# Performance work log

Hardware: AMD Instinct MI355X
Metric: run time of the kernel (lower is better)

The kernel has to match this reference:

```python
import jax, jax.numpy as jnp
import numpy as np

D = 512
H = 8
DH = D // H
SPK = 4
HG = 128  # max(16, D//4)
EPS = 1e-5


def _layernorm(x, gamma, beta):
    mu = jnp.mean(x, axis=-1, keepdims=True)
    var = jnp.var(x, axis=-1, keepdims=True)
    return (x - mu) * jax.lax.rsqrt(var + EPS) * gamma + beta


def setup_inputs() -> dict:
    key = jax.random.key(0)
    ks = jax.random.split(key, 16)
    B, T = 8, 4096
    s = 0.02
    return {
        'token_emb': jax.random.normal(ks[0], (B, T, D), jnp.float32),
        'speaker_emb': jax.random.normal(ks[1], (B, D), jnp.float32),
        'We': jax.random.normal(ks[2], (D * SPK, D), jnp.float32) * s,
        'be': jnp.zeros((D * SPK,), jnp.float32),
        'spk_pos': jax.random.normal(ks[3], (1, SPK, D), jnp.float32) * s,
        'Wq': jax.random.normal(ks[4], (D, D), jnp.float32) * s,
        'bq': jnp.zeros((D,), jnp.float32),
        'Wk': jax.random.normal(ks[5], (D, D), jnp.float32) * s,
        'bk': jnp.zeros((D,), jnp.float32),
        'Wv': jax.random.normal(ks[6], (D, D), jnp.float32) * s,
        'bv': jnp.zeros((D,), jnp.float32),
        'Wo': jax.random.normal(ks[7], (D, D), jnp.float32) * s,
        'bo': jnp.zeros((D,), jnp.float32),
        'gln_gamma': jnp.ones((D,), jnp.float32),
        'gln_beta': jnp.zeros((D,), jnp.float32),
        'Wg1': jax.random.normal(ks[8], (HG, D), jnp.float32) * s,
        'bg1': jnp.zeros((HG,), jnp.float32),
        'Wg2': jax.random.normal(ks[9], (1, HG), jnp.float32) * s,
        'bg2': jnp.zeros((1,), jnp.float32),
        'ln_gamma': jnp.ones((D,), jnp.float32),
        'ln_beta': jnp.zeros((D,), jnp.float32),
    }


def reference(token_emb, speaker_emb, We, be, spk_pos, Wq, bq, Wk, bk, Wv, bv,
              Wo, bo, gln_gamma, gln_beta, Wg1, bg1, Wg2, bg2, ln_gamma, ln_beta):
    B, T, _ = token_emb.shape
    # speaker expansion: (B,D) -> (B, SPK*D) -> (B,SPK,D), plus learned pos
    spk_tokens = jax.nn.relu(speaker_emb @ We.T + be).reshape(B, SPK, D) + spk_pos
    # multi-head cross-attention (batch_first, eval-mode dropout = identity)
    q = (token_emb @ Wq.T + bq).reshape(B, T, H, DH)
    k = (spk_tokens @ Wk.T + bk).reshape(B, SPK, H, DH)
    v = (spk_tokens @ Wv.T + bv).reshape(B, SPK, H, DH)
    scores = jnp.einsum('bthd,bshd->bhts', q, k) / jnp.sqrt(jnp.float32(DH))
    w = jax.nn.softmax(scores, axis=-1)  # (B,H,T,SPK)
    ctx = jnp.einsum('bhts,bshd->bthd', w, v).reshape(B, T, D)
    attn_output = ctx @ Wo.T + bo
    attn_weights = jnp.mean(w, axis=1)  # torch MHA averages heads -> (B,T,SPK)
    # gate: LN -> Linear -> ReLU -> Linear -> Sigmoid
    g = _layernorm(token_emb, gln_gamma, gln_beta)
    g = jax.nn.relu(g @ Wg1.T + bg1)
    g_used = jax.nn.sigmoid(g @ Wg2.T + bg2)  # (B,T,1)
    # residual + final LayerNorm (dropout identity in eval)
    fused = _layernorm(token_emb + g_used * attn_output, ln_gamma, ln_beta)
    return (fused, attn_weights, g_used)
```

## Files before the change

kernel.cpp:

```cpp
#include <hip/hip_runtime.h>
#include <hip/hip_bf16.h>
#include <stdint.h>

typedef __attribute__((ext_vector_type(8))) short short8;
typedef __attribute__((ext_vector_type(4))) short short4v;
typedef __attribute__((ext_vector_type(4))) float f32x4;
typedef __attribute__((ext_vector_type(2))) unsigned int uint2v;

#define DD 512
#define TT 16
#define TN 4096
#define NB 8

__device__ __forceinline__ unsigned short f2bf(float f){
  uint32_t u = __float_as_uint(f);
  u += 0x7FFFu + ((u >> 16) & 1u);
  return (unsigned short)(u >> 16);
}
__device__ __forceinline__ float bf2f(unsigned short h){
  return __uint_as_float(((uint32_t)h) << 16);
}


__global__ void prep_spk(const float* __restrict__ se, const float* __restrict__ We,
                         const float* __restrict__ be, const float* __restrict__ spos,
                         float* __restrict__ spk){
  int idx = blockIdx.x * 256 + threadIdx.x;
  int sub = idx & 15; int out = idx >> 4;
  int b = out & 7, od = out >> 3;
  const float* wr = We + (size_t)od * DD + sub * 4;
  const float* sb = se + b * DD + sub * 4;
  float acc = 0.f;
#pragma unroll
  for (int i = 0; i < 8; i++){
    float4 w = *(const float4*)(wr + i * 64);
    float4 x = *(const float4*)(sb + i * 64);
    acc += w.x * x.x + w.y * x.y + w.z * x.z + w.w * x.w;
  }
  acc += __shfl_xor(acc, 1); acc += __shfl_xor(acc, 2);
  acc += __shfl_xor(acc, 4); acc += __shfl_xor(acc, 8);
  if (sub == 0) spk[b * 2048 + od] = fmaxf(acc + be[od], 0.f) + spos[od];
}

__global__ void prep_kv(const float* __restrict__ spk, const float* __restrict__ Wk,
                        const float* __restrict__ bk, const float* __restrict__ Wv,
                        const float* __restrict__ bv, float* __restrict__ kb,
                        float* __restrict__ vb){
  int idx = blockIdx.x * 256 + threadIdx.x;
  int sub = idx & 15; int out = idx >> 4;
  int hd = out >> 5; int r = out & 31; int b = r >> 2, s = r & 3;
  const float* sp  = spk + (b * 4 + s) * DD + sub * 4;
  const float* wkr = Wk + (size_t)hd * DD + sub * 4;
  const float* wvr = Wv + (size_t)hd * DD + sub * 4;
  float ak = 0.f, av = 0.f;
#pragma unroll
  for (int i = 0; i < 8; i++){
    float4 x  = *(const float4*)(sp + i * 64);
    float4 wk = *(const float4*)(wkr + i * 64);
    float4 wv = *(const float4*)(wvr + i * 64);
    ak += x.x * wk.x + x.y * wk.y + x.z * wk.z + x.w * wk.w;
    av += x.x * wv.x + x.y * wv.y + x.z * wv.z + x.w * wv.w;
  }
  ak += __shfl_xor(ak, 1); ak += __shfl_xor(ak, 2);
  ak += __shfl_xor(ak, 4); ak += __shfl_xor(ak, 8);
  av += __shfl_xor(av, 1); av += __shfl_xor(av, 2);
  av += __shfl_xor(av, 4); av += __shfl_xor(av, 8);
  if (sub == 0){
    kb[(b * 4 + s) * DD + hd] = ak + bk[hd];
    vb[(b * 4 + s) * DD + hd] = av + bv[hd];
  }
}

__global__ void prep_mu(const float* __restrict__ kb, const float* __restrict__ vb,
                        const float* __restrict__ Wq, const float* __restrict__ bq,
                        const float* __restrict__ Wo, const float* __restrict__ bo,
                        const float* __restrict__ Wg1,
                        const float* __restrict__ glng, const float* __restrict__ glnb,
                        const float* __restrict__ bg1,
                        unsigned short* __restrict__ mS, unsigned short* __restrict__ uS,
                        float* __restrict__ cArr, unsigned short* __restrict__ wg1S,
                        float* __restrict__ e1, float* __restrict__ e2){
  int idx = blockIdx.x * 256 + threadIdx.x;
  if (idx < 131072){
    int d = idx & 511; int j = (idx >> 9) & 31; int b = idx >> 14;
    int h = j >> 2, s = j & 3;
    const float* kr = kb + (b * 4 + s) * DD + h * 64;
    const float* wq = Wq + (size_t)(h * 64) * DD + d;
    float acc = 0.f;
#pragma unroll 16
    for (int dh = 0; dh < 64; dh++) acc += wq[(size_t)dh * DD] * kr[dh];
    int kt = d >> 5, kgp = (d >> 3) & 3, e = d & 7;
    int half = j >> 4;
    mS[(size_t)(b * 16 + kt) * 1024 + half * 512 + (kgp * 16 + (j & 15)) * 8 + e] = f2bf(acc);
  } else if (idx < 262144){
    int t = idx - 131072;
    int j = t & 31; int d = (t >> 5) & 511; int b = t >> 14;
    int h = j >> 2, s = j & 3;
    const float* vr = vb + (b * 4 + s) * DD + h * 64;
    const float* wo = Wo + (size_t)d * DD + h * 64;
    float acc = 0.f;
#pragma unroll 8
    for (int dh = 0; dh < 64; dh += 4){
      float4 v4 = *(const float4*)(vr + dh);
      float4 w4 = *(const float4*)(wo + dh);
      acc += v4.x * w4.x + v4.y * w4.y + v4.z * w4.z + v4.w * w4.w;
    }
    int nc = d >> 7, nt = (d >> 4) & 7, r16p = d & 15;
    int kgp = j >> 3, e = j & 7;
    uS[(size_t)(b * 32 + nc * 8 + nt) * 512 + (kgp * 16 + r16p) * 8 + e] =
        f2bf(acc + bo[d] * 0.125f);
  } else if (idx < 327680){
    int t = idx - 262144;
    int col = t >> 9, d = t & 511;
    int nt = col >> 4, c16 = col & 15;
    int kt = d >> 5, kgp = (d >> 3) & 3, e = d & 7;
    wg1S[(size_t)(nt * 16 + kt) * 512 + (kgp * 16 + c16) * 8 + e] = f2bf(Wg1[t] * glng[d]);
  } else if (idx < 327936){
    int t = idx - 327680; int j = t & 31, b = t >> 5;
    int h = j >> 2, s = j & 3;
    const float* kr = kb + (b * 4 + s) * DD + h * 64;
    const float* bqp = bq + h * 64;
    float acc = 0.f;
    for (int dh = 0; dh < 64; dh++) acc += bqp[dh] * kr[dh];
    cArr[b * 32 + j] = acc;
  } else if (idx < 328064){
    int col = idx - 327936;
    const float* wr = Wg1 + (size_t)col * DD;
    float a1 = 0.f, a2 = 0.f;
    for (int d = 0; d < DD; d += 4){
      float4 w  = *(const float4*)(wr + d);
      float4 gm = *(const float4*)(glng + d);
      float4 bt = *(const float4*)(glnb + d);
      a1 += w.x * gm.x + w.y * gm.y + w.z * gm.z + w.w * gm.w;
      a2 += w.x * bt.x + w.y * bt.y + w.z * bt.z + w.w * bt.w;
    }
    e1[col] = a1; e2[col] = a2 + bg1[col];
  }
}


__global__ __launch_bounds__(64) void fused_main(
    const float* __restrict__ xin,
    const float* __restrict__ e1v, const float* __restrict__ e2v,
    const float* __restrict__ wg2v, const float* __restrict__ bg2v,
    const float* __restrict__ lng, const float* __restrict__ lnb,
    const unsigned short* __restrict__ mS,
    const unsigned short* __restrict__ uS,
    const float* __restrict__ cArr,
    const unsigned short* __restrict__ wg1S,
    float* __restrict__ outF, float* __restrict__ outAW, float* __restrict__ outG)
{
  __shared__ __align__(16) unsigned short Yb[TT * DD];
  __shared__ __align__(16) unsigned short Wl[TT * 32];

  const int lane = threadIdx.x;
  const int r16 = lane & 15;
  const int kg  = lane >> 4;
  const int bb  = blockIdx.x >> 8;
  const int t0  = (blockIdx.x & 255) << 4;
  const size_t rowbase = (size_t)bb * TN + t0;
  const int swzS = (r16 & 7) << 3;

  const float* xbase = xin + rowbase * DD;
  float4 xl[32];
#pragma unroll
  for (int i = 0; i < 32; i++){
    const int r = i >> 1;
    xl[i] = *(const float4*)(xbase + r * DD + (i & 1) * 256 + lane * 4);
  }
#pragma unroll
  for (int i = 0; i < 32; i++){
    const int r = i >> 1;
    const int col = (i & 1) * 256 + lane * 4;
    short4v pk;
    pk[0] = (short)f2bf(xl[i].x); pk[1] = (short)f2bf(xl[i].y);
    pk[2] = (short)f2bf(xl[i].z); pk[3] = (short)f2bf(xl[i].w);
    *(short4v*)&Yb[r * DD + (col ^ ((r & 7) << 3))] = pk;
  }
  __syncthreads();

  short8 af[16];
  float s = 0.f, q = 0.f;
#pragma unroll
  for (int kt = 0; kt < 16; kt++){
    af[kt] = *(const short8*)&Yb[r16 * DD + ((kt * 32 + kg * 8) ^ swzS)];
#pragma unroll
    for (int j = 0; j < 8; j++){
      float v = bf2f((unsigned short)af[kt][j]);
      s += v; q += v * v;
    }
  }
  s += __shfl_xor(s, 16); s += __shfl_xor(s, 32);
  q += __shfl_xor(q, 16); q += __shfl_xor(q, 32);
  const float mu = s * (1.f / DD);
  const float rs = rsqrtf(q * (1.f / DD) - mu * mu + 1e-5f);

  const unsigned short* mSp = mS + (size_t)bb * 16384;
  f32x4 sa0 = {0.f,0.f,0.f,0.f}, sa1 = {0.f,0.f,0.f,0.f};
  f32x4 gacc[8];
#pragma unroll
  for (int nt = 0; nt < 8; nt++){ f32x4 z = {0.f,0.f,0.f,0.f}; gacc[nt] = z; }
#pragma unroll
  for (int kt = 0; kt < 16; kt++){
    short8 b0 = *(const short8*)(mSp + (size_t)kt * 1024 + lane * 8);
    short8 b1 = *(const short8*)(mSp + (size_t)kt * 1024 + 512 + lane * 8);
    sa0 = __builtin_amdgcn_mfma_f32_16x16x32_bf16(af[kt], b0, sa0, 0, 0, 0);
    sa1 = __builtin_amdgcn_mfma_f32_16x16x32_bf16(af[kt], b1, sa1, 0, 0, 0);
#pragma unroll
    for (int nt = 0; nt < 8; nt++){
      short8 wf = *(const short8*)(wg1S + (size_t)(nt * 16 + kt) * 512 + lane * 8);
      gacc[nt] = __builtin_amdgcn_mfma_f32_16x16x32_bf16(wf, af[kt], gacc[nt], 0, 0, 0);
    }
  }

  float4 e1c[8], e2c[8], w2c[8];
#pragma unroll
  for (int nt = 0; nt < 8; nt++){
    const int c4 = nt * 16 + kg * 4;
    e1c[nt] = *(const float4*)(e1v + c4);
    e2c[nt] = *(const float4*)(e2v + c4);
    w2c[nt] = *(const float4*)(wg2v + c4);
  }
  const float c0v  = cArr[bb * 32 + r16];
  const float c1v  = cArr[bb * 32 + r16 + 16];
  const float bg2s = bg2v[0];

#pragma unroll
  for (int r = 0; r < 4; r++){
    float s0 = (sa0[r] + c0v) * 0.125f;
    float s1 = (sa1[r] + c1v) * 0.125f;
    float mx0 = fmaxf(s0, __shfl_xor(s0, 1)); mx0 = fmaxf(mx0, __shfl_xor(mx0, 2));
    float mx1 = fmaxf(s1, __shfl_xor(s1, 1)); mx1 = fmaxf(mx1, __shfl_xor(mx1, 2));
    float e0 = __expf(s0 - mx0), e1x = __expf(s1 - mx1);
    float d0 = e0;  d0 += __shfl_xor(d0, 1); d0 += __shfl_xor(d0, 2);
    float d1 = e1x; d1 += __shfl_xor(d1, 1); d1 += __shfl_xor(d1, 2);
    float w0 = e0 / d0, w1 = e1x / d1;
    float t = w0 + w1; t += __shfl_xor(t, 4); t += __shfl_xor(t, 8); t *= 0.125f;
    const int rw = kg * 4 + r;
    if ((lane & 12) == 0) outAW[(rowbase + rw) * 4 + (lane & 3)] = t;
    Wl[rw * 32 + r16]      = f2bf(w0);
    Wl[rw * 32 + r16 + 16] = f2bf(w1);
  }

  short8 aw = *(const short8*)&Wl[r16 * 32 + kg * 8];
  const unsigned short* uSp = uS + (size_t)bb * 16384;
  const int c0 = lane << 3;
  float4 lgA0 = *(const float4*)(lng + c0);
  float4 lgA1 = *(const float4*)(lng + c0 + 4);
  float4 lbA0 = *(const float4*)(lnb + c0);
  float4 lbA1 = *(const float4*)(lnb + c0 + 4);

  float g_reg;
  {
    float part = 0.f;
#pragma unroll
    for (int nt = 0; nt < 8; nt++){
      float e1a[4] = {e1c[nt].x, e1c[nt].y, e1c[nt].z, e1c[nt].w};
      float e2a[4] = {e2c[nt].x, e2c[nt].y, e2c[nt].z, e2c[nt].w};
      float w2a[4] = {w2c[nt].x, w2c[nt].y, w2c[nt].z, w2c[nt].w};
#pragma unroll
      for (int r = 0; r < 4; r++){
        float gv = rs * (gacc[nt][r] - mu * e1a[r]) + e2a[r];
        gv = fmaxf(gv, 0.f);
        part += gv * w2a[r];
      }
    }
    part += __shfl_xor(part, 16); part += __shfl_xor(part, 32);
    g_reg = 1.f / (1.f + __expf(-(part + bg2s)));
    if (kg == 0) outG[rowbase + r16] = g_reg;
  }

  float psum = 0.f, psq = 0.f;
#pragma unroll
  for (int nc = 0; nc < 4; nc++){
    f32x4 acc[8];
#pragma unroll
    for (int nt = 0; nt < 8; nt++){
      short8 uf = *(const short8*)(uSp + (size_t)(nc * 8 + nt) * 512 + lane * 8);
      f32x4 z = {0.f,0.f,0.f,0.f};
      acc[nt] = __builtin_amdgcn_mfma_f32_16x16x32_bf16(uf, aw, z, 0, 0, 0);
    }
#pragma unroll
    for (int nt = 0; nt < 8; nt++){
      const int idx = r16 * DD + ((nc * 128 + nt * 16 + kg * 4) ^ swzS);
      uint2v xch = *(const uint2v*)&Yb[idx];
      unsigned int lo = xch[0], hi = xch[1];
      float y0 = bf2f((unsigned short)(lo & 0xffffu)) + g_reg * acc[nt][0];
      float y1 = bf2f((unsigned short)(lo >> 16))     + g_reg * acc[nt][1];
      float y2 = bf2f((unsigned short)(hi & 0xffffu)) + g_reg * acc[nt][2];
      float y3 = bf2f((unsigned short)(hi >> 16))     + g_reg * acc[nt][3];
      psum += (y0 + y1) + (y2 + y3);
      psq  += (y0 * y0 + y1 * y1) + (y2 * y2 + y3 * y3);
      uint2v yp;
      yp[0] = (unsigned)f2bf(y0) | ((unsigned)f2bf(y1) << 16);
      yp[1] = (unsigned)f2bf(y2) | ((unsigned)f2bf(y3) << 16);
      *(uint2v*)&Yb[idx] = yp;
    }
  }

  psum += __shfl_xor(psum, 16); psum += __shfl_xor(psum, 32);
  psq  += __shfl_xor(psq, 16);  psq  += __shfl_xor(psq, 32);
  const float mu2 = psum * (1.f / DD);
  const float rs2 = rsqrtf(psq * (1.f / DD) - mu2 * mu2 + 1e-5f);

  float lg[8]  = {lgA0.x, lgA0.y, lgA0.z, lgA0.w, lgA1.x, lgA1.y, lgA1.z, lgA1.w};
  float lb8[8] = {lbA0.x, lbA0.y, lbA0.z, lbA0.w, lbA1.x, lbA1.y, lbA1.z, lbA1.w};
#pragma unroll
  for (int r = 0; r < TT; r++){
    const float m2  = __shfl(mu2, r);
    const float r2v = __shfl(rs2, r);
    short8 yv = *(const short8*)&Yb[r * DD + (c0 ^ ((r & 7) << 3))];
    float o[8];
#pragma unroll
    for (int j = 0; j < 8; j++)
      o[j] = (bf2f((unsigned short)yv[j]) - m2) * r2v * lg[j] + lb8[j];
    float* op = outF + (rowbase + r) * DD + c0;
    float4 o0; o0.x = o[0]; o0.y = o[1]; o0.z = o[2]; o0.w = o[3];
    float4 o1; o1.x = o[4]; o1.y = o[5]; o1.z = o[6]; o1.w = o[7];
    *(float4*)op = o0;
    *(float4*)(op + 4) = o1;
  }
}


extern "C" void kernel_launch(void* const* d_in, const int* in_sizes, int n_in,
                              void* d_out, int out_size, void* d_ws, size_t ws_size,
                              hipStream_t stream)
{
  const float* token = (const float*)d_in[0];
  const float* semb  = (const float*)d_in[1];
  const float* We    = (const float*)d_in[2];
  const float* be    = (const float*)d_in[3];
  const float* spos  = (const float*)d_in[4];
  const float* Wq    = (const float*)d_in[5];
  const float* bq    = (const float*)d_in[6];
  const float* Wk    = (const float*)d_in[7];
  const float* bk    = (const float*)d_in[8];
  const float* Wv    = (const float*)d_in[9];
  const float* bv    = (const float*)d_in[10];
  const float* Wo    = (const float*)d_in[11];
  const float* bo    = (const float*)d_in[12];
  const float* glng  = (const float*)d_in[13];
  const float* glnb  = (const float*)d_in[14];
  const float* Wg1   = (const float*)d_in[15];
  const float* bg1   = (const float*)d_in[16];
  const float* Wg2   = (const float*)d_in[17];
  const float* bg2   = (const float*)d_in[18];
  const float* lng   = (const float*)d_in[19];
  const float* lnb   = (const float*)d_in[20];

  char* ws = (char*)d_ws;
  float* e1             = (float*)(ws + 0);
  float* e2             = (float*)(ws + 512);
  float* spk            = (float*)(ws + 0);
  float* kb             = (float*)(ws + 65536);
  float* vb             = (float*)(ws + 131072);
  unsigned short* mS    = (unsigned short*)(ws + 196608);
  unsigned short* uS    = (unsigned short*)(ws + 458752);
  float* cArr           = (float*)(ws + 720896);
  unsigned short* wg1S  = (unsigned short*)(ws + 721920);

  float* outF  = (float*)d_out;
  float* outAW = outF + (size_t)NB * TN * DD;
  float* outG  = outAW + (size_t)NB * TN * 4;

  prep_spk<<<dim3(1024), dim3(256), 0, stream>>>(semb, We, be, spos, spk);
  prep_kv<<<dim3(1024), dim3(256), 0, stream>>>(spk, Wk, bk, Wv, bv, kb, vb);
  prep_mu<<<dim3(1282), dim3(256), 0, stream>>>(kb, vb, Wq, bq, Wo, bo, Wg1, glng, glnb, bg1,
                                                mS, uS, cArr, wg1S, e1, e2);
  fused_main<<<dim3(NB * TN / TT), dim3(64), 0, stream>>>(
      token, e1, e2, Wg2, bg2, lng, lnb,
      mS, uS, cArr, wg1S, outF, outAW, outG);
}
```

Before: 71.58 us.

## Split fused main kernel across four waves and merge prep kernels

The main kernel moves from one 64-thread wave per 16-token tile to four waves. The waves share the score, gate and Wo-projection MFMAs, and LayerNorm statistics are combined through shared memory with extra barriers. The three prep kernels become two: speaker expansion, K/V projection and the bias dot run in 32 blocks using shared memory, and the Wg1 packing is done per wave. The goal is less serial work and fewer registers per wave (the old xl[32] and af[16] arrays are gone) so occupancy rises, at the cost of more syncs and shared-memory traffic per block.

```diff
diff --git a/kernel.cpp b/kernel.cpp
--- a/kernel.cpp
+++ b/kernel.cpp
@@ -22,64 +22,101 @@
 }
 
 
-__global__ void prep_spk(const float* __restrict__ se, const float* __restrict__ We,
-                         const float* __restrict__ be, const float* __restrict__ spos,
-                         float* __restrict__ spk){
-  int idx = blockIdx.x * 256 + threadIdx.x;
-  int sub = idx & 15; int out = idx >> 4;
-  int b = out & 7, od = out >> 3;
-  const float* wr = We + (size_t)od * DD + sub * 4;
-  const float* sb = se + b * DD + sub * 4;
-  float acc = 0.f;
-#pragma unroll
-  for (int i = 0; i < 8; i++){
-    float4 w = *(const float4*)(wr + i * 64);
-    float4 x = *(const float4*)(sb + i * 64);
-    acc += w.x * x.x + w.y * x.y + w.z * x.z + w.w * x.w;
-  }
-  acc += __shfl_xor(acc, 1); acc += __shfl_xor(acc, 2);
-  acc += __shfl_xor(acc, 4); acc += __shfl_xor(acc, 8);
-  if (sub == 0) spk[b * 2048 + od] = fmaxf(acc + be[od], 0.f) + spos[od];
-}
-
-__global__ void prep_kv(const float* __restrict__ spk, const float* __restrict__ Wk,
-                        const float* __restrict__ bk, const float* __restrict__ Wv,
-                        const float* __restrict__ bv, float* __restrict__ kb,
-                        float* __restrict__ vb){
-  int idx = blockIdx.x * 256 + threadIdx.x;
-  int sub = idx & 15; int out = idx >> 4;
-  int hd = out >> 5; int r = out & 31; int b = r >> 2, s = r & 3;
-  const float* sp  = spk + (b * 4 + s) * DD + sub * 4;
-  const float* wkr = Wk + (size_t)hd * DD + sub * 4;
-  const float* wvr = Wv + (size_t)hd * DD + sub * 4;
-  float ak = 0.f, av = 0.f;
-#pragma unroll
-  for (int i = 0; i < 8; i++){
-    float4 x  = *(const float4*)(sp + i * 64);
-    float4 wk = *(const float4*)(wkr + i * 64);
-    float4 wv = *(const float4*)(wvr + i * 64);
-    ak += x.x * wk.x + x.y * wk.y + x.z * wk.z + x.w * wk.w;
-    av += x.x * wv.x + x.y * wv.y + x.z * wv.z + x.w * wv.w;
-  }
-  ak += __shfl_xor(ak, 1); ak += __shfl_xor(ak, 2);
-  ak += __shfl_xor(ak, 4); ak += __shfl_xor(ak, 8);
-  av += __shfl_xor(av, 1); av += __shfl_xor(av, 2);
-  av += __shfl_xor(av, 4); av += __shfl_xor(av, 8);
-  if (sub == 0){
-    kb[(b * 4 + s) * DD + hd] = ak + bk[hd];
-    vb[(b * 4 + s) * DD + hd] = av + bv[hd];
-  }
-}
-
-__global__ void prep_mu(const float* __restrict__ kb, const float* __restrict__ vb,
-                        const float* __restrict__ Wq, const float* __restrict__ bq,
-                        const float* __restrict__ Wo, const float* __restrict__ bo,
-                        const float* __restrict__ Wg1,
-                        const float* __restrict__ glng, const float* __restrict__ glnb,
-                        const float* __restrict__ bg1,
-                        unsigned short* __restrict__ mS, unsigned short* __restrict__ uS,
-                        float* __restrict__ cArr, unsigned short* __restrict__ wg1S,
-                        float* __restrict__ e1, float* __restrict__ e2){
+__global__ __launch_bounds__(256) void prep_a(
+    const float* __restrict__ se, const float* __restrict__ We,
+    const float* __restrict__ be, const float* __restrict__ spos,
+    const float* __restrict__ Wk, const float* __restrict__ bk,
+    const float* __restrict__ Wv, const float* __restrict__ bv,
+    const float* __restrict__ bq, const float* __restrict__ Wg1,
+    const float* __restrict__ glng, const float* __restrict__ glnb,
+    const float* __restrict__ bg1,
+    float* __restrict__ kb, float* __restrict__ vb,
+    float* __restrict__ cArr, unsigned short* __restrict__ wg1S,
+    float* __restrict__ e1, float* __restrict__ e2)
+{
+  const int blk = blockIdx.x, tid = threadIdx.x;
+  if (blk < 32){
+    __shared__ float spk_loc[512];
+    __shared__ float k_loc[512], v_loc[512];
+    const int b = blk >> 2, s = blk & 3;
+    const int sub = tid & 3, o0 = tid >> 2;
+    const float* sb = se + b * DD + sub * 4;
+#pragma unroll
+    for (int pass = 0; pass < 8; ++pass){
+      const int o = pass * 64 + o0;
+      const float* wr = We + (size_t)(s * DD + o) * DD + sub * 4;
+      float acc = 0.f;
+#pragma unroll
+      for (int i = 0; i < 32; ++i){
+        float4 w4 = *(const float4*)(wr + i * 16);
+        float4 x4 = *(const float4*)(sb + i * 16);
+        acc += w4.x*x4.x + w4.y*x4.y + w4.z*x4.z + w4.w*x4.w;
+      }
+      acc += __shfl_xor(acc, 1); acc += __shfl_xor(acc, 2);
+      if (sub == 0) spk_loc[o] = fmaxf(acc + be[s*DD+o], 0.f) + spos[s*DD+o];
+    }
+    __syncthreads();
+#pragma unroll
+    for (int pass = 0; pass < 8; ++pass){
+      const int hd = pass * 64 + o0;
+      const float* wkr = Wk + (size_t)hd * DD + sub * 4;
+      const float* wvr = Wv + (size_t)hd * DD + sub * 4;
+      float ak = 0.f, av = 0.f;
+#pragma unroll
+      for (int i = 0; i < 32; ++i){
+        float4 x4  = *(const float4*)(&spk_loc[sub*4 + i*16]);
+        float4 wk4 = *(const float4*)(wkr + i * 16);
+        float4 wv4 = *(const float4*)(wvr + i * 16);
+        ak += x4.x*wk4.x + x4.y*wk4.y + x4.z*wk4.z + x4.w*wk4.w;
+        av += x4.x*wv4.x + x4.y*wv4.y + x4.z*wv4.z + x4.w*wv4.w;
+      }
+      ak += __shfl_xor(ak, 1); ak += __shfl_xor(ak, 2);
+      av += __shfl_xor(av, 1); av += __shfl_xor(av, 2);
+      if (sub == 0){
+        const float kk = ak + bk[hd], vv = av + bv[hd];
+        k_loc[hd] = kk; v_loc[hd] = vv;
+        kb[(b*4+s)*DD + hd] = kk; vb[(b*4+s)*DD + hd] = vv;
+      }
+    }
+    __syncthreads();
+    if (tid < 8){
+      float acc = 0.f;
+      for (int dh = 0; dh < 64; ++dh) acc += bq[tid*64+dh] * k_loc[tid*64+dh];
+      cArr[b*32 + tid*4 + s] = acc;
+    }
+  } else {
+    const int wv = tid >> 6, lane = tid & 63;
+    const int col = (blk - 32) * 4 + wv;
+    const float* wr = Wg1 + (size_t)col * DD + lane * 8;
+    float4 w0 = *(const float4*)wr, w1 = *(const float4*)(wr + 4);
+    float4 g0 = *(const float4*)(glng + lane*8), g1 = *(const float4*)(glng + lane*8 + 4);
+    float4 b0 = *(const float4*)(glnb + lane*8), b1 = *(const float4*)(glnb + lane*8 + 4);
+    float wa[8] = {w0.x,w0.y,w0.z,w0.w,w1.x,w1.y,w1.z,w1.w};
+    float ga[8] = {g0.x,g0.y,g0.z,g0.w,g1.x,g1.y,g1.z,g1.w};
+    float ba[8] = {b0.x,b0.y,b0.z,b0.w,b1.x,b1.y,b1.z,b1.w};
+    float p1 = 0.f, p2 = 0.f;
+    short8 st;
+#pragma unroll
+    for (int j = 0; j < 8; ++j){
+      p1 += wa[j]*ga[j]; p2 += wa[j]*ba[j];
+      st[j] = (short)f2bf(wa[j]*ga[j]);
+    }
+    *(short8*)&wg1S[((size_t)((col>>4)*16 + (lane>>2)))*512 + ((lane&3)*16 + (col&15))*8] = st;
+#pragma unroll
+    for (int off = 1; off < 64; off <<= 1){
+      p1 += __shfl_xor(p1, off); p2 += __shfl_xor(p2, off);
+    }
+    if (lane == 0){ e1[col] = p1; e2[col] = p2 + bg1[col]; }
+  }
+}
+
+
+__global__ __launch_bounds__(256) void prep_b(
+    const float* __restrict__ kb, const float* __restrict__ vb,
+    const float* __restrict__ Wq, const float* __restrict__ Wo,
+    const float* __restrict__ bo,
+    unsigned short* __restrict__ mS, unsigned short* __restrict__ uS)
+{
   int idx = blockIdx.x * 256 + threadIdx.x;
   if (idx < 131072){
     int d = idx & 511; int j = (idx >> 9) & 31; int b = idx >> 14;
@@ -92,7 +129,7 @@
     int kt = d >> 5, kgp = (d >> 3) & 3, e = d & 7;
     int half = j >> 4;
     mS[(size_t)(b * 16 + kt) * 1024 + half * 512 + (kgp * 16 + (j & 15)) * 8 + e] = f2bf(acc);
-  } else if (idx < 262144){
+  } else {
     int t = idx - 131072;
     int j = t & 31; int d = (t >> 5) & 511; int b = t >> 14;
     int h = j >> 2, s = j & 3;
@@ -109,37 +146,11 @@
     int kgp = j >> 3, e = j & 7;
     uS[(size_t)(b * 32 + nc * 8 + nt) * 512 + (kgp * 16 + r16p) * 8 + e] =
         f2bf(acc + bo[d] * 0.125f);
-  } else if (idx < 327680){
-    int t = idx - 262144;
-    int col = t >> 9, d = t & 511;
-    int nt = col >> 4, c16 = col & 15;
-    int kt = d >> 5, kgp = (d >> 3) & 3, e = d & 7;
-    wg1S[(size_t)(nt * 16 + kt) * 512 + (kgp * 16 + c16) * 8 + e] = f2bf(Wg1[t] * glng[d]);
-  } else if (idx < 327936){
-    int t = idx - 327680; int j = t & 31, b = t >> 5;
-    int h = j >> 2, s = j & 3;
-    const float* kr = kb + (b * 4 + s) * DD + h * 64;
-    const float* bqp = bq + h * 64;
-    float acc = 0.f;
-    for (int dh = 0; dh < 64; dh++) acc += bqp[dh] * kr[dh];
-    cArr[b * 32 + j] = acc;
-  } else if (idx < 328064){
-    int col = idx - 327936;
-    const float* wr = Wg1 + (size_t)col * DD;
-    float a1 = 0.f, a2 = 0.f;
-    for (int d = 0; d < DD; d += 4){
-      float4 w  = *(const float4*)(wr + d);
-      float4 gm = *(const float4*)(glng + d);
-      float4 bt = *(const float4*)(glnb + d);
-      a1 += w.x * gm.x + w.y * gm.y + w.z * gm.z + w.w * gm.w;
-      a2 += w.x * bt.x + w.y * bt.y + w.z * bt.z + w.w * bt.w;
-    }
-    e1[col] = a1; e2[col] = a2 + bg1[col];
-  }
-}
-
-
-__global__ __launch_bounds__(64) void fused_main(
+  }
+}
+
+
+__global__ __launch_bounds__(256, 4) void fused_main(
     const float* __restrict__ xin,
     const float* __restrict__ e1v, const float* __restrict__ e2v,
     const float* __restrict__ wg2v, const float* __restrict__ bg2v,
@@ -152,173 +163,192 @@
 {
   __shared__ __align__(16) unsigned short Yb[TT * DD];
   __shared__ __align__(16) unsigned short Wl[TT * 32];
-
-  const int lane = threadIdx.x;
-  const int r16 = lane & 15;
-  const int kg  = lane >> 4;
-  const int bb  = blockIdx.x >> 8;
-  const int t0  = (blockIdx.x & 255) << 4;
+  __shared__ float smu[TT], srs[TT];
+  __shared__ float aws[2][64];
+  __shared__ float gp[4][TT];
+  __shared__ float pp[4][TT], qq[4][TT];
+
+  const int tid  = threadIdx.x;
+  const int w    = tid >> 6;
+  const int lane = tid & 63;
+  const int r16  = lane & 15;
+  const int kg   = lane >> 4;
+  const int bb   = blockIdx.x >> 8;
+  const int t0   = (blockIdx.x & 255) << 4;
   const size_t rowbase = (size_t)bb * TN + t0;
   const int swzS = (r16 & 7) << 3;
 
   const float* xbase = xin + rowbase * DD;
-  float4 xl[32];
-#pragma unroll
-  for (int i = 0; i < 32; i++){
-    const int r = i >> 1;
-    xl[i] = *(const float4*)(xbase + r * DD + (i & 1) * 256 + lane * 4);
-  }
-#pragma unroll
-  for (int i = 0; i < 32; i++){
-    const int r = i >> 1;
-    const int col = (i & 1) * 256 + lane * 4;
-    short4v pk;
-    pk[0] = (short)f2bf(xl[i].x); pk[1] = (short)f2bf(xl[i].y);
-    pk[2] = (short)f2bf(xl[i].z); pk[3] = (short)f2bf(xl[i].w);
-    *(short4v*)&Yb[r * DD + (col ^ ((r & 7) << 3))] = pk;
+#pragma unroll
+  for (int i = 0; i < 4; ++i){
+    const int rr = w * 4 + i;
+    const int swz = (rr & 7) << 3;
+    float s = 0.f, q = 0.f;
+#pragma unroll
+    for (int h2 = 0; h2 < 2; ++h2){
+      const int col = h2 * 256 + lane * 4;
+      float4 v4 = *(const float4*)(xbase + rr * DD + col);
+      float xv[4] = {v4.x, v4.y, v4.z, v4.w};
+      short4v pk;
+#pragma unroll
+      for (int j = 0; j < 4; ++j){ s += xv[j]; q += xv[j]*xv[j]; pk[j] = (short)f2bf(xv[j]); }
+      *(short4v*)&Yb[rr * DD + (col ^ swz)] = pk;
+    }
+#pragma unroll
+    for (int off = 1; off < 64; off <<= 1){ s += __shfl_xor(s, off); q += __shfl_xor(q, off); }
+    if (lane == 0){
+      const float mu = s * (1.f/DD);
+      smu[rr] = mu;
+      srs[rr] = rsqrtf(q * (1.f/DD) - mu*mu + 1e-5f);
+    }
   }
   __syncthreads();
 
-  short8 af[16];
-  float s = 0.f, q = 0.f;
-#pragma unroll
-  for (int kt = 0; kt < 16; kt++){
-    af[kt] = *(const short8*)&Yb[r16 * DD + ((kt * 32 + kg * 8) ^ swzS)];
-#pragma unroll
-    for (int j = 0; j < 8; j++){
-      float v = bf2f((unsigned short)af[kt][j]);
-      s += v; q += v * v;
-    }
-  }
-  s += __shfl_xor(s, 16); s += __shfl_xor(s, 32);
-  q += __shfl_xor(q, 16); q += __shfl_xor(q, 32);
-  const float mu = s * (1.f / DD);
-  const float rs = rsqrtf(q * (1.f / DD) - mu * mu + 1e-5f);
-
-  const unsigned short* mSp = mS + (size_t)bb * 16384;
-  f32x4 sa0 = {0.f,0.f,0.f,0.f}, sa1 = {0.f,0.f,0.f,0.f};
-  f32x4 gacc[8];
-#pragma unroll
-  for (int nt = 0; nt < 8; nt++){ f32x4 z = {0.f,0.f,0.f,0.f}; gacc[nt] = z; }
-#pragma unroll
-  for (int kt = 0; kt < 16; kt++){
-    short8 b0 = *(const short8*)(mSp + (size_t)kt * 1024 + lane * 8);
-    short8 b1 = *(const short8*)(mSp + (size_t)kt * 1024 + 512 + lane * 8);
-    sa0 = __builtin_amdgcn_mfma_f32_16x16x32_bf16(af[kt], b0, sa0, 0, 0, 0);
-    sa1 = __builtin_amdgcn_mfma_f32_16x16x32_bf16(af[kt], b1, sa1, 0, 0, 0);
-#pragma unroll
-    for (int nt = 0; nt < 8; nt++){
-      short8 wf = *(const short8*)(wg1S + (size_t)(nt * 16 + kt) * 512 + lane * 8);
-      gacc[nt] = __builtin_amdgcn_mfma_f32_16x16x32_bf16(wf, af[kt], gacc[nt], 0, 0, 0);
-    }
-  }
-
-  float4 e1c[8], e2c[8], w2c[8];
-#pragma unroll
-  for (int nt = 0; nt < 8; nt++){
-    const int c4 = nt * 16 + kg * 4;
-    e1c[nt] = *(const float4*)(e1v + c4);
-    e2c[nt] = *(const float4*)(e2v + c4);
-    w2c[nt] = *(const float4*)(wg2v + c4);
-  }
-  const float c0v  = cArr[bb * 32 + r16];
-  const float c1v  = cArr[bb * 32 + r16 + 16];
+  const int half = w & 1;
+  const int nt0 = w * 2;
+  const unsigned short* mSp  = mS + (size_t)bb * 16384 + half * 512 + lane * 8;
+  const unsigned short* wgp0 = wg1S + (size_t)(nt0 * 16) * 512 + lane * 8;
+  const unsigned short* wgp1 = wgp0 + (size_t)16 * 512;
+  f32x4 sa = {0.f,0.f,0.f,0.f}, ga0 = {0.f,0.f,0.f,0.f}, ga1 = {0.f,0.f,0.f,0.f};
+  if (w < 2){
+#pragma unroll
+    for (int kt = 0; kt < 16; ++kt){
+      short8 af = *(const short8*)&Yb[r16 * DD + ((kt*32 + kg*8) ^ swzS)];
+      short8 b0 = *(const short8*)(mSp + (size_t)kt * 1024);
+      sa  = __builtin_amdgcn_mfma_f32_16x16x32_bf16(af, b0, sa, 0, 0, 0);
+      short8 wf0 = *(const short8*)(wgp0 + (size_t)kt * 512);
+      ga0 = __builtin_amdgcn_mfma_f32_16x16x32_bf16(wf0, af, ga0, 0, 0, 0);
+      short8 wf1 = *(const short8*)(wgp1 + (size_t)kt * 512);
+      ga1 = __builtin_amdgcn_mfma_f32_16x16x32_bf16(wf1, af, ga1, 0, 0, 0);
+    }
+  } else {
+#pragma unroll
+    for (int kt = 0; kt < 16; ++kt){
+      short8 af = *(const short8*)&Yb[r16 * DD + ((kt*32 + kg*8) ^ swzS)];
+      short8 wf0 = *(const short8*)(wgp0 + (size_t)kt * 512);
+      ga0 = __builtin_amdgcn_mfma_f32_16x16x32_bf16(wf0, af, ga0, 0, 0, 0);
+      short8 wf1 = *(const short8*)(wgp1 + (size_t)kt * 512);
+      ga1 = __builtin_amdgcn_mfma_f32_16x16x32_bf16(wf1, af, ga1, 0, 0, 0);
+    }
+  }
+
+  float4 e1c[2], e2c[2], w2c[2];
+#pragma unroll
+  for (int t = 0; t < 2; ++t){
+    const int c4 = (nt0 + t) * 16 + kg * 4;
+    e1c[t] = *(const float4*)(e1v + c4);
+    e2c[t] = *(const float4*)(e2v + c4);
+    w2c[t] = *(const float4*)(wg2v + c4);
+  }
+  float4 lgh[2], lbh[2];
+#pragma unroll
+  for (int h2 = 0; h2 < 2; ++h2){
+    lgh[h2] = *(const float4*)(lng + h2*256 + lane*4);
+    lbh[h2] = *(const float4*)(lnb + h2*256 + lane*4);
+  }
   const float bg2s = bg2v[0];
 
-#pragma unroll
-  for (int r = 0; r < 4; r++){
-    float s0 = (sa0[r] + c0v) * 0.125f;
-    float s1 = (sa1[r] + c1v) * 0.125f;
-    float mx0 = fmaxf(s0, __shfl_xor(s0, 1)); mx0 = fmaxf(mx0, __shfl_xor(mx0, 2));
-    float mx1 = fmaxf(s1, __shfl_xor(s1, 1)); mx1 = fmaxf(mx1, __shfl_xor(mx1, 2));
-    float e0 = __expf(s0 - mx0), e1x = __expf(s1 - mx1);
-    float d0 = e0;  d0 += __shfl_xor(d0, 1); d0 += __shfl_xor(d0, 2);
-    float d1 = e1x; d1 += __shfl_xor(d1, 1); d1 += __shfl_xor(d1, 2);
-    float w0 = e0 / d0, w1 = e1x / d1;
-    float t = w0 + w1; t += __shfl_xor(t, 4); t += __shfl_xor(t, 8); t *= 0.125f;
-    const int rw = kg * 4 + r;
-    if ((lane & 12) == 0) outAW[(rowbase + rw) * 4 + (lane & 3)] = t;
-    Wl[rw * 32 + r16]      = f2bf(w0);
-    Wl[rw * 32 + r16 + 16] = f2bf(w1);
-  }
-
-  short8 aw = *(const short8*)&Wl[r16 * 32 + kg * 8];
-  const unsigned short* uSp = uS + (size_t)bb * 16384;
-  const int c0 = lane << 3;
-  float4 lgA0 = *(const float4*)(lng + c0);
-  float4 lgA1 = *(const float4*)(lng + c0 + 4);
-  float4 lbA0 = *(const float4*)(lnb + c0);
-  float4 lbA1 = *(const float4*)(lnb + c0 + 4);
-
+  if (w < 2){
+    const float cv = cArr[bb*32 + half*16 + r16];
+#pragma unroll
+    for (int r = 0; r < 4; ++r){
+      float s0 = (sa[r] + cv) * 0.125f;
+      float mx = fmaxf(s0, __shfl_xor(s0, 1)); mx = fmaxf(mx, __shfl_xor(mx, 2));
+      float e0 = __expf(s0 - mx);
+      float d0 = e0; d0 += __shfl_xor(d0, 1); d0 += __shfl_xor(d0, 2);
+      float wv = e0 / d0;
+      float t = wv; t += __shfl_xor(t, 4); t += __shfl_xor(t, 8);
+      const int rw = kg * 4 + r;
+      Wl[rw * 32 + half * 16 + r16] = f2bf(wv);
+      if ((lane & 12) == 0) aws[half][rw * 4 + (lane & 3)] = t;
+    }
+  }
+
+  {
+    const float mu_t = smu[r16], rs_t = srs[r16];
+    float part = 0.f;
+#pragma unroll
+    for (int t = 0; t < 2; ++t){
+      const f32x4 ga = t ? ga1 : ga0;
+      float ea[4] = {e1c[t].x, e1c[t].y, e1c[t].z, e1c[t].w};
+      float eb[4] = {e2c[t].x, e2c[t].y, e2c[t].z, e2c[t].w};
+      float wc[4] = {w2c[t].x, w2c[t].y, w2c[t].z, w2c[t].w};
+#pragma unroll
+      for (int r = 0; r < 4; ++r){
+        float gv = rs_t * (ga[r] - mu_t * ea[r]) + eb[r];
+        part += fmaxf(gv, 0.f) * wc[r];
+      }
+    }
+    part += __shfl_xor(part, 16); part += __shfl_xor(part, 32);
+    if (kg == 0) gp[w][r16] = part;
+  }
+  __syncthreads();
+
+  if (w == 2){
+    const int tok = lane >> 2;
+    const float val = (aws[0][lane] + aws[1][lane]) * 0.125f;
+    outAW[(rowbase + tok) * 4 + (lane & 3)] = val;
+  }
   float g_reg;
   {
-    float part = 0.f;
-#pragma unroll
-    for (int nt = 0; nt < 8; nt++){
-      float e1a[4] = {e1c[nt].x, e1c[nt].y, e1c[nt].z, e1c[nt].w};
-      float e2a[4] = {e2c[nt].x, e2c[nt].y, e2c[nt].z, e2c[nt].w};
-      float w2a[4] = {w2c[nt].x, w2c[nt].y, w2c[nt].z, w2c[nt].w};
-#pragma unroll
-      for (int r = 0; r < 4; r++){
-        float gv = rs * (gacc[nt][r] - mu * e1a[r]) + e2a[r];
-        gv = fmaxf(gv, 0.f);
-        part += gv * w2a[r];
-      }
-    }
-    part += __shfl_xor(part, 16); part += __shfl_xor(part, 32);
-    g_reg = 1.f / (1.f + __expf(-(part + bg2s)));
-    if (kg == 0) outG[rowbase + r16] = g_reg;
-  }
-
+    const float gs = gp[0][r16] + gp[1][r16] + gp[2][r16] + gp[3][r16];
+    g_reg = 1.f / (1.f + __expf(-(gs + bg2s)));
+    if (w == 3 && kg == 0) outG[rowbase + r16] = g_reg;
+  }
+
+  short8 awf = *(const short8*)&Wl[r16 * 32 + kg * 8];
+  const unsigned short* uSp = uS + (size_t)bb * 16384 + (size_t)(w * 8) * 512 + lane * 8;
+  f32x4 acc[8];
+#pragma unroll
+  for (int nt = 0; nt < 8; ++nt){
+    short8 uf = *(const short8*)(uSp + (size_t)nt * 512);
+    f32x4 z = {0.f,0.f,0.f,0.f};
+    acc[nt] = __builtin_amdgcn_mfma_f32_16x16x32_bf16(uf, awf, z, 0, 0, 0);
+  }
   float psum = 0.f, psq = 0.f;
 #pragma unroll
-  for (int nc = 0; nc < 4; nc++){
-    f32x4 acc[8];
-#pragma unroll
-    for (int nt = 0; nt < 8; nt++){
-      short8 uf = *(const short8*)(uSp + (size_t)(nc * 8 + nt) * 512 + lane * 8);
-      f32x4 z = {0.f,0.f,0.f,0.f};
-      acc[nt] = __builtin_amdgcn_mfma_f32_16x16x32_bf16(uf, aw, z, 0, 0, 0);
-    }
-#pragma unroll
-    for (int nt = 0; nt < 8; nt++){
-      const int idx = r16 * DD + ((nc * 128 + nt * 16 + kg * 4) ^ swzS);
-      uint2v xch = *(const uint2v*)&Yb[idx];
-      unsigned int lo = xch[0], hi = xch[1];
-      float y0 = bf2f((unsigned short)(lo & 0xffffu)) + g_reg * acc[nt][0];
-      float y1 = bf2f((unsigned short)(lo >> 16))     + g_reg * acc[nt][1];
-      float y2 = bf2f((unsigned short)(hi & 0xffffu)) + g_reg * acc[nt][2];
-      float y3 = bf2f((unsigned short)(hi >> 16))     + g_reg * acc[nt][3];
-      psum += (y0 + y1) + (y2 + y3);
-      psq  += (y0 * y0 + y1 * y1) + (y2 * y2 + y3 * y3);
-      uint2v yp;
-      yp[0] = (unsigned)f2bf(y0) | ((unsigned)f2bf(y1) << 16);
-      yp[1] = (unsigned)f2bf(y2) | ((unsigned)f2bf(y3) << 16);
-      *(uint2v*)&Yb[idx] = yp;
-    }
-  }
-
+  for (int nt = 0; nt < 8; ++nt){
+    const int c4 = w * 128 + nt * 16 + kg * 4;
+    const int idx = r16 * DD + (c4 ^ swzS);
+    uint2v xch = *(const uint2v*)&Yb[idx];
+    unsigned int lo = xch[0], hi = xch[1];
+    float y0 = bf2f((unsigned short)(lo & 0xffffu)) + g_reg * acc[nt][0];
+    float y1 = bf2f((unsigned short)(lo >> 16))     + g_reg * acc[nt][1];
+    float y2 = bf2f((unsigned short)(hi & 0xffffu)) + g_reg * acc[nt][2];
+    float y3 = bf2f((unsigned short)(hi >> 16))     + g_reg * acc[nt][3];
+    psum += (y0 + y1) + (y2 + y3);
+    psq  += (y0*y0 + y1*y1) + (y2*y2 + y3*y3);
+    uint2v yp;
+    yp[0] = (unsigned)f2bf(y0) | ((unsigned)f2bf(y1) << 16);
+    yp[1] = (unsigned)f2bf(y2) | ((unsigned)f2bf(y3) << 16);
+    *(uint2v*)&Yb[idx] = yp;
+  }
   psum += __shfl_xor(psum, 16); psum += __shfl_xor(psum, 32);
   psq  += __shfl_xor(psq, 16);  psq  += __shfl_xor(psq, 32);
-  const float mu2 = psum * (1.f / DD);
-  const float rs2 = rsqrtf(psq * (1.f / DD) - mu2 * mu2 + 1e-5f);
-
-  float lg[8]  = {lgA0.x, lgA0.y, lgA0.z, lgA0.w, lgA1.x, lgA1.y, lgA1.z, lgA1.w};
-  float lb8[8] = {lbA0.x, lbA0.y, lbA0.z, lbA0.w, lbA1.x, lbA1.y, lbA1.z, lbA1.w};
-#pragma unroll
-  for (int r = 0; r < TT; r++){
-    const float m2  = __shfl(mu2, r);
-    const float r2v = __shfl(rs2, r);
-    short8 yv = *(const short8*)&Yb[r * DD + (c0 ^ ((r & 7) << 3))];
-    float o[8];
-#pragma unroll
-    for (int j = 0; j < 8; j++)
-      o[j] = (bf2f((unsigned short)yv[j]) - m2) * r2v * lg[j] + lb8[j];
-    float* op = outF + (rowbase + r) * DD + c0;
-    float4 o0; o0.x = o[0]; o0.y = o[1]; o0.z = o[2]; o0.w = o[3];
-    float4 o1; o1.x = o[4]; o1.y = o[5]; o1.z = o[6]; o1.w = o[7];
-    *(float4*)op = o0;
-    *(float4*)(op + 4) = o1;
+  if (kg == 0){ pp[w][r16] = psum; qq[w][r16] = psq; }
+  __syncthreads();
+
+#pragma unroll
+  for (int i = 0; i < 4; ++i){
+    const int rr = w * 4 + i;
+    const float sm = pp[0][rr] + pp[1][rr] + pp[2][rr] + pp[3][rr];
+    const float sq = qq[0][rr] + qq[1][rr] + qq[2][rr] + qq[3][rr];
+    const float mu2 = sm * (1.f/DD);
+    const float rs2 = rsqrtf(sq * (1.f/DD) - mu2*mu2 + 1e-5f);
+    const int swz = (rr & 7) << 3;
+#pragma unroll
+    for (int h2 = 0; h2 < 2; ++h2){
+      const int col = h2 * 256 + lane * 4;
+      short4v yv = *(const short4v*)&Yb[rr * DD + (col ^ swz)];
+      float la[4] = {lgh[h2].x, lgh[h2].y, lgh[h2].z, lgh[h2].w};
+      float lb4[4] = {lbh[h2].x, lbh[h2].y, lbh[h2].z, lbh[h2].w};
+      float4 o;
+      o.x = (bf2f((unsigned short)yv[0]) - mu2) * rs2 * la[0] + lb4[0];
+      o.y = (bf2f((unsigned short)yv[1]) - mu2) * rs2 * la[1] + lb4[1];
+      o.z = (bf2f((unsigned short)yv[2]) - mu2) * rs2 * la[2] + lb4[2];
+      o.w = (bf2f((unsigned short)yv[3]) - mu2) * rs2 * la[3] + lb4[3];
+      *(float4*)(outF + (rowbase + rr) * DD + col) = o;
+    }
   }
 }
 
@@ -352,7 +382,6 @@
   char* ws = (char*)d_ws;
   float* e1             = (float*)(ws + 0);
   float* e2             = (float*)(ws + 512);
-  float* spk            = (float*)(ws + 0);
   float* kb             = (float*)(ws + 65536);
   float* vb             = (float*)(ws + 131072);
   unsigned short* mS    = (unsigned short*)(ws + 196608);
@@ -364,11 +393,11 @@
   float* outAW = outF + (size_t)NB * TN * DD;
   float* outG  = outAW + (size_t)NB * TN * 4;
 
-  prep_spk<<<dim3(1024), dim3(256), 0, stream>>>(semb, We, be, spos, spk);
-  prep_kv<<<dim3(1024), dim3(256), 0, stream>>>(spk, Wk, bk, Wv, bv, kb, vb);
-  prep_mu<<<dim3(1282), dim3(256), 0, stream>>>(kb, vb, Wq, bq, Wo, bo, Wg1, glng, glnb, bg1,
-                                                mS, uS, cArr, wg1S, e1, e2);
-  fused_main<<<dim3(NB * TN / TT), dim3(64), 0, stream>>>(
+  prep_a<<<dim3(64), dim3(256), 0, stream>>>(semb, We, be, spos, Wk, bk, Wv, bv, bq,
+                                             Wg1, glng, glnb, bg1,
+                                             kb, vb, cArr, wg1S, e1, e2);
+  prep_b<<<dim3(1024), dim3(256), 0, stream>>>(kb, vb, Wq, Wo, bo, mS, uS);
+  fused_main<<<dim3(NB * TN / TT), dim3(256), 0, stream>>>(
       token, e1, e2, Wg2, bg2, lng, lnb,
       mS, uS, cArr, wg1S, outF, outAW, outG);
 }
```

After: 142.4 us. 1.99x slower.
